# Optimization experiments

Hardware: AMD Instinct MI355X
Metric: run time of the kernel (lower is better)

The kernel has to match this reference:

```python
import jax, jax.numpy as jnp
import numpy as np

N, K, D = 32768, 8192, 512

def setup_inputs() -> dict:
    key = jax.random.key(0)
    kx, kw = jax.random.split(key)
    x = jax.random.normal(kx, (N, D), dtype=jnp.float32)
    # nn.Embedding weight init: uniform(-1/K, 1/K)
    codebook = jax.random.uniform(kw, (K, D), dtype=jnp.float32, minval=-1.0 / K, maxval=1.0 / K)
    return {"x": x, "codebook": codebook}

def reference(x, codebook):
    distances = (
        jnp.sum(x * x, axis=1, keepdims=True)
        + jnp.sum(codebook * codebook, axis=1)
        - 2.0 * jnp.einsum("nd,kd->nk", x, codebook)
    )
    encoding_indices = jnp.argmin(distances, axis=1)            # [N]
    encodings = jax.nn.one_hot(encoding_indices, K, dtype=x.dtype)  # [N, K]
    quantized = jnp.einsum("nk,kd->nd", encodings, codebook)    # [N, D]
    return quantized, encodings, encoding_indices
```

## Files before the change

kernel.cpp:

```cpp
#include <hip/hip_runtime.h>
#include <hip/hip_fp8.h>
#include <stdint.h>

#define D     512
#define BM    128
#define BN    128
#define BKC   128
#define CAND  64
#define MARGIN 7e-4f
#define MARGINS (8192.0f * MARGIN)
#define KDIM  8192

typedef __attribute__((ext_vector_type(4))) float f32x4;
typedef unsigned long long u64;

__device__ __forceinline__ unsigned char f2fp8(float f) {
  __hip_fp8_e4m3 q(f);
  return (unsigned char)q.__x;
}

__device__ __forceinline__ unsigned fkey(float f) {
  unsigned u = __float_as_uint(f);
  return (u >> 31) ? ~u : (u | 0x80000000u);
}
__device__ __forceinline__ float unfkey(unsigned k) {
  unsigned u = (k >> 31) ? (k & 0x7FFFFFFFu) : ~k;
  return __uint_as_float(u);
}

__global__ __launch_bounds__(256) void vq_prep(const float* __restrict__ cb,
                                               unsigned char* __restrict__ w8,
                                               float* __restrict__ b32, int K) {
  int wid  = blockIdx.x * 4 + (threadIdx.x >> 6);
  int lane = threadIdx.x & 63;
  if (wid >= K) return;
  const float* row = cb + (size_t)wid * D + lane * 8;
  float4 a = *(const float4*)row;
  float4 b = *(const float4*)(row + 4);
  float v[8] = {a.x, a.y, a.z, a.w, b.x, b.y, b.z, b.w};
  double s = 0.0;
  u64 p = 0ull;
#pragma unroll
  for (int j = 0; j < 8; ++j) {
    float sq = v[j] * v[j]; s += (double)sq;
    p |= (u64)f2fp8(v[j] * 8192.0f) << (8 * j);
  }
  *(u64*)(w8 + (size_t)wid * D + lane * 8) = p;
#pragma unroll
  for (int m = 1; m < 64; m <<= 1) s += __shfl_xor(s, m);
  if (lane == 0) b32[wid] = (float)s;
}

__device__ __forceinline__ void stage2(const unsigned char* __restrict__ w8,
                                       unsigned char (*wb)[BN * BKC], int kt2, int c2,
                                       int w, int lane) {
#pragma unroll
  for (int i = 0; i < 2; ++i) {
    const int sb  = (w * 2 + i) * 64;
    const int s   = sb + lane;
    const int row = s >> 3;
    const int j   = s & 7;
    const int k16 = j ^ (row & 7);
    const unsigned char* src = w8 + (size_t)(kt2 * BN + row) * D + c2 * BKC + k16 * 16;
    unsigned char* dst = &wb[c2][sb * 16];
    __builtin_amdgcn_global_load_lds(
        (const __attribute__((address_space(1))) unsigned int*)src,
        (__attribute__((address_space(3))) unsigned int*)dst, 16, 0, 0);
  }
}

__global__ __launch_bounds__(512, 2) void vq_main(
    const float* __restrict__ x, const float* __restrict__ cb,
    const unsigned char* __restrict__ w8, const float* __restrict__ b32g,
    float* __restrict__ out_q, float* __restrict__ out_enc, float* __restrict__ out_idx,
    int N, int K) {
  __shared__ unsigned char wb[4][BN * BKC];
  __shared__ unsigned rowmin[BM];
  __shared__ unsigned rowcnt[BM];
  __shared__ u64 candb[BM][CAND];

  const int t    = threadIdx.x;
  const int lane = t & 63;
  const int w    = t >> 6;
  const int wr   = w >> 1;
  const int wc   = w & 1;
  const int l15  = lane & 15;
  const int l16  = lane >> 4;
  const int m_base = blockIdx.x * BM;
  const int nkt  = K / BN;
  float* const enc_blk = out_enc + (size_t)m_base * K;

  if (t < BM) { rowmin[t] = 0xFFFFFFFFu; rowcnt[t] = 0u; }

  stage2(w8, wb, 0, 0, w, lane);
  stage2(w8, wb, 0, 1, w, lane);

  long afr[2][16];
#pragma unroll
  for (int mi = 0; mi < 2; ++mi) {
    const float* xr = x + (size_t)(m_base + 32 * wr + 16 * mi + l15) * D;
#pragma unroll
    for (int f = 0; f < 16; ++f) {
      const float* p = xr + f * 32 + l16 * 8;
      float4 a = *(const float4*)p;
      float4 b = *(const float4*)(p + 4);
      float v[8] = {a.x, a.y, a.z, a.w, b.x, b.y, b.z, b.w};
      u64 pk = 0ull;
#pragma unroll
      for (int j = 0; j < 8; ++j) pk |= (u64)f2fp8(v[j]) << (8 * j);
      afr[mi][f] = (long)pk;
    }
  }
  __syncthreads();

  for (int kt = 0; kt < nkt; ++kt) {
    float b32v[4];
#pragma unroll
    for (int ni = 0; ni < 4; ++ni)
      b32v[ni] = 8192.0f * b32g[kt * BN + 64 * wc + 16 * ni + l15];

    f32x4 acc[2][4];
#pragma unroll
    for (int mi = 0; mi < 2; ++mi)
#pragma unroll
      for (int ni = 0; ni < 4; ++ni) acc[mi][ni] = (f32x4){0.f, 0.f, 0.f, 0.f};

#pragma unroll
    for (int c = 0; c < 4; ++c) {
      const int kt2 = kt + ((c + 2) >> 2);
      if (kt2 < nkt) stage2(w8, wb, kt2, (c + 2) & 3, w, lane);
      {
        const f32x4 z4 = {0.f, 0.f, 0.f, 0.f};
        f32x4* ez = (f32x4*)(enc_blk + (size_t)kt * (BM * KDIM / 64));
        __builtin_nontemporal_store(z4, ez + (c * 2 + 0) * 512 + t);
        __builtin_nontemporal_store(z4, ez + (c * 2 + 1) * 512 + t);
      }

      const unsigned char* wp = &wb[c][0];
      __builtin_amdgcn_s_setprio(1);
#pragma unroll
      for (int ks = 0; ks < 4; ++ks) {
        long bfr[4];
#pragma unroll
        for (int ni = 0; ni < 4; ++ni) {
          const int row  = 64 * wc + 16 * ni + l15;
          const int slot = (ks * 2 + (l16 >> 1)) ^ (row & 7);
          bfr[ni] = *(const long*)(wp + row * BKC + slot * 16 + (l16 & 1) * 8);
        }
#pragma unroll
        for (int mi = 0; mi < 2; ++mi)
#pragma unroll
          for (int ni = 0; ni < 4; ++ni)
            acc[mi][ni] = __builtin_amdgcn_mfma_f32_16x16x32_fp8_fp8(
                afr[mi][c * 4 + ks], bfr[ni], acc[mi][ni], 0, 0, 0);
      }
      __builtin_amdgcn_s_setprio(0);
      if (kt2 < nkt) asm volatile("s_waitcnt vmcnt(6)" ::: "memory");
      else           asm volatile("s_waitcnt vmcnt(0)" ::: "memory");
      __builtin_amdgcn_sched_barrier(0);
      __builtin_amdgcn_s_barrier();
    }

    float tv[2][4][4];
#pragma unroll
    for (int mi = 0; mi < 2; ++mi)
#pragma unroll
      for (int ni = 0; ni < 4; ++ni)
#pragma unroll
        for (int r = 0; r < 4; ++r)
          tv[mi][ni][r] = fmaf(-2.0f, acc[mi][ni][r], b32v[ni]);

    if (kt == 0) {
#pragma unroll
      for (int mi = 0; mi < 2; ++mi)
#pragma unroll
        for (int r = 0; r < 4; ++r) {
          float m = fminf(fminf(tv[mi][0][r], tv[mi][1][r]),
                          fminf(tv[mi][2][r], tv[mi][3][r]));
          atomicMin(&rowmin[32 * wr + 16 * mi + 4 * l16 + r], fkey(m));
        }
      __syncthreads();
    }

#pragma unroll
    for (int mi = 0; mi < 2; ++mi) {
      const int rbase = 32 * wr + 16 * mi + 4 * l16;
      const uint4 ru = *(const uint4*)&rowmin[rbase];
      const unsigned rua[4] = {ru.x, ru.y, ru.z, ru.w};
#pragma unroll
      for (int r = 0; r < 4; ++r) {
        const float rm  = unfkey(rua[r]);
        const float thr = rm + MARGINS;
        const float mn  = fminf(fminf(tv[mi][0][r], tv[mi][1][r]),
                                fminf(tv[mi][2][r], tv[mi][3][r]));
        if (mn < rm) atomicMin(&rowmin[rbase + r], fkey(mn));
#pragma unroll
        for (int ni = 0; ni < 4; ++ni) {
          if (tv[mi][ni][r] <= thr) {
            unsigned p = atomicAdd(&rowcnt[rbase + r], 1u);
            if (p < CAND)
              candb[rbase + r][p] = ((u64)fkey(tv[mi][ni][r]) << 32)
                                  | (unsigned)(kt * BN + 64 * wc + 16 * ni + l15);
          }
        }
      }
    }
  }
  __syncthreads();

  for (int r = w; r < BM; r += 8) {
    const int n = m_base + r;
    const float* xr = x + (size_t)n * D + l15 * 32;
    float xv[32];
#pragma unroll
    for (int j4 = 0; j4 < 8; ++j4) {
      float4 v = *(const float4*)(xr + j4 * 4);
      xv[j4 * 4 + 0] = v.x; xv[j4 * 4 + 1] = v.y;
      xv[j4 * 4 + 2] = v.z; xv[j4 * 4 + 3] = v.w;
    }
    double s = 0.0;
#pragma unroll
    for (int j = 0; j < 32; ++j) { float sq = xv[j] * xv[j]; s += (double)sq; }
#pragma unroll
    for (int m = 1; m < 16; m <<= 1) s += __shfl_xor(s, m);
    const float Arow = (float)s;

    const unsigned cgot = rowcnt[r];
    const bool uselist = (cgot >= 1u && cgot <= (unsigned)CAND);
    const int nc = uselist ? (int)cgot : K;
    const float thrF = unfkey(rowmin[r]) + MARGINS;
    u64 best = 0xFFFFFFFFFFFFFFFFull;

    for (int i = 0; i < nc; i += 4) {
      const int ci = i + l16;
      if (ci < nc) {
        int k; bool ok = true;
        if (uselist) {
          const u64 e = candb[r][ci];
          k = (int)(e & 0xFFFFFFFFu);
          ok = (unfkey((unsigned)(e >> 32)) <= thrF);
        } else k = ci;
        if (ok) {
          const float* wp = cb + (size_t)k * D + l15 * 32;
          double d = 0.0;
#pragma unroll
          for (int j4 = 0; j4 < 8; ++j4) {
            float4 v = *(const float4*)(wp + j4 * 4);
            d += (double)xv[j4 * 4 + 0] * v.x; d += (double)xv[j4 * 4 + 1] * v.y;
            d += (double)xv[j4 * 4 + 2] * v.z; d += (double)xv[j4 * 4 + 3] * v.w;
          }
#pragma unroll
          for (int m = 1; m < 16; m <<= 1) d += __shfl_xor(d, m);
          const float C32 = (float)d;
          const float T1  = Arow + b32g[k];
          const float sc  = T1 - 2.0f * C32;
          const u64 pk = ((u64)__float_as_uint(sc) << 32) | (unsigned)k;
          best = best < pk ? best : pk;
        }
      }
    }
    {
      u64 o = __shfl_xor(best, 16); best = best < o ? best : o;
      o     = __shfl_xor(best, 32); best = best < o ? best : o;
    }
    const int kstar = (int)(best & 0xFFFFFFFFu);

    if (lane == 0) {
      out_idx[n] = (float)kstar;
      out_enc[(size_t)n * K + kstar] = 1.0f;
    }
    const float* qs = cb + (size_t)kstar * D + lane * 8;
    float4 q0 = *(const float4*)qs;
    float4 q1 = *(const float4*)(qs + 4);
    f32x4* qd = (f32x4*)(out_q + (size_t)n * D + lane * 8);
    f32x4 q0v = {q0.x, q0.y, q0.z, q0.w};
    f32x4 q1v = {q1.x, q1.y, q1.z, q1.w};
    __builtin_nontemporal_store(q0v, qd);
    __builtin_nontemporal_store(q1v, qd + 1);
  }
}

extern "C" void kernel_launch(void* const* d_in, const int* in_sizes, int n_in,
                              void* d_out, int out_size, void* d_ws, size_t ws_size,
                              hipStream_t stream) {
  const float* x  = (const float*)d_in[0];
  const float* cb = (const float*)d_in[1];
  const int N = in_sizes[0] / D;
  const int K = in_sizes[1] / D;

  unsigned char* w8 = (unsigned char*)d_ws;
  float* b32 = (float*)((char*)d_ws + (size_t)K * D);

  float* out     = (float*)d_out;
  float* out_q   = out;
  float* out_enc = out + (size_t)N * D;
  float* out_idx = out + (size_t)N * D + (size_t)N * K;

  vq_prep<<<(K + 3) / 4, 256, 0, stream>>>(cb, w8, b32, K);
  vq_main<<<N / BM, 512, 0, stream>>>(x, cb, w8, b32, out_q, out_enc, out_idx, N, K);
}
```

Measured before the change: 489.5 us.

## Double K-chunk width and switch to three-buffer rotating LDS pipeline

Doubles the per-stage K chunk from 128 to 256 bytes of fp8, so each tile runs two larger stages instead of four. The LDS buffers become a three-slot ring, prefetching two stages ahead, with the XOR swizzle widened to 16 slots and the vmcnt waits adjusted. Candidate capacity is cut from 64 to 56 to fit LDS. The aim is fewer barriers and waits per tile, at the cost of more LDS per stage and a smaller candidate buffer.

```diff
diff --git a/kernel.cpp b/kernel.cpp
--- a/kernel.cpp
+++ b/kernel.cpp
@@ -5,8 +5,8 @@
 #define D     512
 #define BM    128
 #define BN    128
-#define BKC   128
-#define CAND  64
+#define BKC   256
+#define CAND  56
 #define MARGIN 7e-4f
 #define MARGINS (8192.0f * MARGIN)
 #define KDIM  8192
@@ -51,18 +51,18 @@
   if (lane == 0) b32[wid] = (float)s;
 }
 
-__device__ __forceinline__ void stage2(const unsigned char* __restrict__ w8,
-                                       unsigned char (*wb)[BN * BKC], int kt2, int c2,
-                                       int w, int lane) {
-#pragma unroll
-  for (int i = 0; i < 2; ++i) {
-    const int sb  = (w * 2 + i) * 64;
+__device__ __forceinline__ void stage(const unsigned char* __restrict__ w8,
+                                      unsigned char* __restrict__ wbase, int g,
+                                      int buf, int w, int lane) {
+#pragma unroll
+  for (int i = 0; i < 4; ++i) {
+    const int sb  = (w * 4 + i) * 64;
     const int s   = sb + lane;
-    const int row = s >> 3;
-    const int j   = s & 7;
-    const int k16 = j ^ (row & 7);
-    const unsigned char* src = w8 + (size_t)(kt2 * BN + row) * D + c2 * BKC + k16 * 16;
-    unsigned char* dst = &wb[c2][sb * 16];
+    const int row = s >> 4;
+    const int j   = s & 15;
+    const int k16 = j ^ (row & 15);
+    const unsigned char* src = w8 + (size_t)((g >> 1) * BN + row) * D + (g & 1) * BKC + k16 * 16;
+    unsigned char* dst = wbase + buf * (BN * BKC) + sb * 16;
     __builtin_amdgcn_global_load_lds(
         (const __attribute__((address_space(1))) unsigned int*)src,
         (__attribute__((address_space(3))) unsigned int*)dst, 16, 0, 0);
@@ -74,7 +74,7 @@
     const unsigned char* __restrict__ w8, const float* __restrict__ b32g,
     float* __restrict__ out_q, float* __restrict__ out_enc, float* __restrict__ out_idx,
     int N, int K) {
-  __shared__ unsigned char wb[4][BN * BKC];
+  __shared__ unsigned char wb[3 * BN * BKC];
   __shared__ unsigned rowmin[BM];
   __shared__ unsigned rowcnt[BM];
   __shared__ u64 candb[BM][CAND];
@@ -88,12 +88,13 @@
   const int l16  = lane >> 4;
   const int m_base = blockIdx.x * BM;
   const int nkt  = K / BN;
+  const int ng   = 2 * nkt;
   float* const enc_blk = out_enc + (size_t)m_base * K;
 
   if (t < BM) { rowmin[t] = 0xFFFFFFFFu; rowcnt[t] = 0u; }
 
-  stage2(w8, wb, 0, 0, w, lane);
-  stage2(w8, wb, 0, 1, w, lane);
+  stage(w8, wb, 0, 0, w, lane);
+  stage(w8, wb, 1, 1, w, lane);
 
   long afr[2][16];
 #pragma unroll
@@ -113,6 +114,8 @@
   }
   __syncthreads();
 
+  int bufc = 0;
+
   for (int kt = 0; kt < nkt; ++kt) {
     float b32v[4];
 #pragma unroll
@@ -126,25 +129,27 @@
       for (int ni = 0; ni < 4; ++ni) acc[mi][ni] = (f32x4){0.f, 0.f, 0.f, 0.f};
 
 #pragma unroll
-    for (int c = 0; c < 4; ++c) {
-      const int kt2 = kt + ((c + 2) >> 2);
-      if (kt2 < nkt) stage2(w8, wb, kt2, (c + 2) & 3, w, lane);
+    for (int c = 0; c < 2; ++c) {
+      const int g  = kt * 2 + c;
+      const int gp = g + 2;
+      if (gp < ng) stage(w8, wb, gp, (bufc >= 1 ? bufc - 1 : 2), w, lane);
       {
         const f32x4 z4 = {0.f, 0.f, 0.f, 0.f};
         f32x4* ez = (f32x4*)(enc_blk + (size_t)kt * (BM * KDIM / 64));
-        __builtin_nontemporal_store(z4, ez + (c * 2 + 0) * 512 + t);
-        __builtin_nontemporal_store(z4, ez + (c * 2 + 1) * 512 + t);
+#pragma unroll
+        for (int jj = 0; jj < 4; ++jj)
+          __builtin_nontemporal_store(z4, ez + c * 2048 + jj * 512 + t);
       }
 
-      const unsigned char* wp = &wb[c][0];
+      const unsigned char* wp = wb + bufc * (BN * BKC);
       __builtin_amdgcn_s_setprio(1);
 #pragma unroll
-      for (int ks = 0; ks < 4; ++ks) {
+      for (int ks = 0; ks < 8; ++ks) {
         long bfr[4];
 #pragma unroll
         for (int ni = 0; ni < 4; ++ni) {
           const int row  = 64 * wc + 16 * ni + l15;
-          const int slot = (ks * 2 + (l16 >> 1)) ^ (row & 7);
+          const int slot = (ks * 2 + (l16 >> 1)) ^ (row & 15);
           bfr[ni] = *(const long*)(wp + row * BKC + slot * 16 + (l16 & 1) * 8);
         }
 #pragma unroll
@@ -152,13 +157,15 @@
 #pragma unroll
           for (int ni = 0; ni < 4; ++ni)
             acc[mi][ni] = __builtin_amdgcn_mfma_f32_16x16x32_fp8_fp8(
-                afr[mi][c * 4 + ks], bfr[ni], acc[mi][ni], 0, 0, 0);
+                afr[mi][c * 8 + ks], bfr[ni], acc[mi][ni], 0, 0, 0);
       }
       __builtin_amdgcn_s_setprio(0);
-      if (kt2 < nkt) asm volatile("s_waitcnt vmcnt(6)" ::: "memory");
-      else           asm volatile("s_waitcnt vmcnt(0)" ::: "memory");
+      if (gp < ng)          asm volatile("s_waitcnt vmcnt(12)" ::: "memory");
+      else if (g + 1 < ng)  asm volatile("s_waitcnt vmcnt(4)"  ::: "memory");
+      else                  asm volatile("s_waitcnt vmcnt(0)"  ::: "memory");
       __builtin_amdgcn_sched_barrier(0);
       __builtin_amdgcn_s_barrier();
+      bufc = (bufc >= 2) ? 0 : bufc + 1;
     }
 
     float tv[2][4][4];
```

Measured after the change: 565.4 us. +15.5%, slower.
